# Kernel optimization log

Hardware: AMD Instinct MI355X
Metric: run time of the kernel (lower is better)

The kernel has to match this reference:

```python
import jax, jax.numpy as jnp
import numpy as np

KSIZE = 7
HEAD_DIM = 64
EPS = 1e-6

def rmsnorm(x, w):
    return x * jax.lax.rsqrt(jnp.mean(x * x, axis=-1, keepdims=True) + EPS) * w

def rope2d(x):
    # Split channels: first half rotated by row position, second half by column position.
    B, H, W, C = x.shape
    half = C // 2
    q = half // 2
    inv = 1.0 / (10000.0 ** (jnp.arange(q, dtype=jnp.float32) / q))
    th_y = jnp.arange(H, dtype=jnp.float32)[:, None] * inv  # [H,q]
    th_x = jnp.arange(W, dtype=jnp.float32)[:, None] * inv  # [W,q]
    def rot(v, th):  # v: [...,q,2], th broadcastable to [...,q]
        c, s = jnp.cos(th), jnp.sin(th)
        a, b = v[..., 0], v[..., 1]
        return jnp.stack([a * c - b * s, a * s + b * c], axis=-1)
    xy = rot(x[..., :half].reshape(B, H, W, q, 2), th_y[None, :, None, :])
    xx = rot(x[..., half:].reshape(B, H, W, q, 2), th_x[None, None, :, :])
    return jnp.concatenate([xy.reshape(B, H, W, half), xx.reshape(B, H, W, half)], axis=-1)

def neighborhood_attn(x, w_qkv, w_proj, b_proj, k=KSIZE, hd=HEAD_DIM):
    # NATTEN semantics: each query attends to a k x k window; window start is
    # clamped at borders so every query sees exactly k*k keys.
    B, H, W, C = x.shape
    nh = C // hd
    qkv = x @ w_qkv                           # [B,H,W,3C]
    qv, kv, vv = jnp.split(qkv, 3, axis=-1)
    qh = qv.reshape(B, H, W, nh, hd)
    kh = kv.reshape(B, H, W, nh, hd)
    vh = vv.reshape(B, H, W, nh, hd)
    idx_h = jnp.clip(jnp.arange(H) - k // 2, 0, H - k)[:, None] + jnp.arange(k)  # [H,k]
    idx_w = jnp.clip(jnp.arange(W) - k // 2, 0, W - k)[:, None] + jnp.arange(k)  # [W,k]
    def gather(t):  # [B,H,W,nh,hd] -> [B,H,W,nh,k*k,hd]
        g = t[:, idx_h]            # [B,H,k,W,nh,hd]
        g = g[:, :, :, idx_w]      # [B,H,k,W,k,nh,hd]
        return g.transpose(0, 1, 3, 5, 2, 4, 6).reshape(B, H, W, nh, k * k, hd)
    kn = gather(kh)
    vn = gather(vh)
    scale = 1.0 / np.sqrt(hd).astype(np.float32)
    logits = jnp.einsum('bxynd,bxynkd->bxynk', qh, kn) * scale
    attn = jax.nn.softmax(logits, axis=-1)
    out = jnp.einsum('bxynk,bxynkd->bxynd', attn, vn).reshape(B, H, W, C)
    return out @ w_proj + b_proj

def geglu(x, ff1_w, ff1_b, ff2_w, ff2_b):
    h = x @ ff1_w + ff1_b
    gate, value = jnp.split(h, 2, axis=-1)
    return (jax.nn.gelu(gate, approximate=False) * value) @ ff2_w + ff2_b

def setup_inputs():
    key = jax.random.key(0)
    B, H, W, C = 2, 64, 64, 256
    ks = jax.random.split(key, 8)
    g = lambda k, shape, sc: jax.random.normal(k, shape, jnp.float32) * sc
    return {
        'x': g(ks[0], (B, H, W, C), 1.0),
        'norm1_w': jnp.ones((C,), jnp.float32),
        'norm2_w': jnp.ones((C,), jnp.float32),
        'w_qkv': g(ks[1], (C, 3 * C), 0.02),
        'w_proj': g(ks[2], (C, C), 0.02),
        'b_proj': g(ks[3], (C,), 0.02),
        'ff1_w': g(ks[4], (C, 2 * C), 0.02),
        'ff1_b': g(ks[5], (2 * C,), 0.02),
        'ff2_w': g(ks[6], (C, C), 0.02),
        'ff2_b': g(ks[7], (C,), 0.02),
    }

def reference(x, norm1_w, norm2_w, w_qkv, w_proj, b_proj, ff1_w, ff1_b, ff2_w, ff2_b):
    h = rope2d(rmsnorm(x, norm1_w))
    x = x + neighborhood_attn(h, w_qkv, w_proj, b_proj)
    x = x + geglu(rmsnorm(x, norm2_w), ff1_w, ff1_b, ff2_w, ff2_b)
    return x
```

## Files before the change

kernel.cpp:

```cpp
#include <hip/hip_runtime.h>
#include <hip/hip_bf16.h>


#define ROWS 8192
typedef unsigned int uint32;
typedef unsigned short ushort16;
typedef __attribute__((ext_vector_type(8))) short short8;
typedef __attribute__((ext_vector_type(4))) float floatx4;

__device__ __forceinline__ float bf2f(__hip_bfloat16 b) { return __bfloat162float(b); }
__device__ __forceinline__ float us2f(ushort16 u) {
    return __uint_as_float(((uint32)u) << 16);
}
__device__ __forceinline__ ushort16 f2us(float f) {
    __hip_bfloat16 h = __float2bfloat16(f);
    return *(ushort16*)&h;
}
__device__ __forceinline__ float ldflag(const void* p, size_t i, int f32) {
    return f32 ? ((const float*)p)[i] : bf2f(((const __hip_bfloat16*)p)[i]);
}

__device__ __forceinline__ void gl_lds16(const void* gptr, void* lptr) {
    __builtin_amdgcn_global_load_lds(
        (const __attribute__((address_space(1))) uint32*)gptr,
        (__attribute__((address_space(3))) uint32*)lptr, 16, 0, 0);
}

__global__ __launch_bounds__(64) void detect_kernel(const ushort16* __restrict__ xu,
                                                    int* __restrict__ flag) {
    const int lane = threadIdx.x;
    const float v = us2f(xu[lane * 62]);
    const float a = fabsf(v);
    const bool sane = (a < 1e4f) && (a > 1e-8f);
    const unsigned long long m = __ballot(sane);
    if (lane == 0) flag[0] = (__popcll(m) < 32) ? 1 : 0;
}

struct WSrc {
    const void *wqkv, *wproj, *ff1w, *ff2w, *bproj, *ff1b, *ff2b;
};
__global__ __launch_bounds__(256) void cvt_kernel(WSrc s, ushort16* __restrict__ wT,
                                                  float* __restrict__ bF,
                                                  const int* __restrict__ flag) {
    const int f32 = flag[0];
    const int bid = blockIdx.x, tid = threadIdx.x;
    if (bid == 112) {
        #pragma unroll
        for (int it = 0; it < 4; ++it) {
            const int j = it * 256 + tid;
            float v;
            if (j < 256)      v = ldflag(s.bproj, j, f32);
            else if (j < 768) v = ldflag(s.ff1b, j - 256, f32);
            else              v = ldflag(s.ff2b, j - 768, f32);
            bF[j] = v;
        }
        return;
    }
    const void* src; int N, kt, nt, base;
    if (bid < 48)      { src = s.wqkv;  N = 768; kt = bid / 12;      nt = bid % 12;      base = 0; }
    else if (bid < 64) { const int l = bid - 48; src = s.wproj; N = 256; kt = l / 4; nt = l % 4; base = 196608; }
    else if (bid < 96) { const int l = bid - 64; src = s.ff1w;  N = 512; kt = l / 8; nt = l % 8; base = 262144; }
    else               { const int l = bid - 96; src = s.ff2w;  N = 256; kt = l / 4; nt = l % 4; base = 393216; }

    __shared__ ushort16 T[64][65];
    const int r0 = tid >> 6, c = tid & 63;
    #pragma unroll
    for (int j = 0; j < 16; ++j) {
        const int r = j * 4 + r0;
        T[r][c] = f2us(ldflag(src, (size_t)(kt * 64 + r) * N + nt * 64 + c, f32));
    }
    __syncthreads();
    const int n = tid >> 2, kg = tid & 3;
    #pragma unroll
    for (int j = 0; j < 16; ++j) {
        const int k = kg * 16 + j;
        wT[base + (size_t)(nt * 64 + n) * 256 + kt * 64 + k] = T[k][n];
    }
}

__global__ __launch_bounds__(256) void rms1_kernel(const void* __restrict__ in,
                                                   const void* __restrict__ w,
                                                   ushort16* __restrict__ out,
                                                   const int* __restrict__ flag) {
    const int f32 = flag[0];
    const int wid = threadIdx.x >> 6, lane = threadIdx.x & 63;
    const int row = blockIdx.x * 4 + wid;
    const int c0 = lane * 4;
    const size_t base = (size_t)row * 256 + c0;

    float v[4];
    if (f32) {
        const float4 d = *(const float4*)((const float*)in + base);
        v[0] = d.x; v[1] = d.y; v[2] = d.z; v[3] = d.w;
    } else {
        const ushort4 d = *(const ushort4*)((const ushort16*)in + base);
        v[0] = us2f(d.x); v[1] = us2f(d.y); v[2] = us2f(d.z); v[3] = us2f(d.w);
    }

    float sq = v[0] * v[0] + v[1] * v[1] + v[2] * v[2] + v[3] * v[3];
    #pragma unroll
    for (int off = 32; off; off >>= 1) sq += __shfl_xor(sq, off);
    const float rr = rsqrtf(sq * (1.0f / 256.0f) + 1e-6f);

    float nv[4];
    #pragma unroll
    for (int i = 0; i < 4; ++i) nv[i] = v[i] * rr * ldflag(w, c0 + i, f32);

    const int py = (row >> 6) & 63, px = row & 63;
    const float pos = (c0 < 128) ? (float)py : (float)px;
    const int j0 = (c0 & 127) >> 1;
    #pragma unroll
    for (int p = 0; p < 2; ++p) {
        const float inv = expf(-(float)(j0 + p) * (9.210340371976184f / 64.0f));
        const float th = pos * inv;
        const float cs = cosf(th), sn = sinf(th);
        const float a = nv[p * 2], b = nv[p * 2 + 1];
        nv[p * 2]     = a * cs - b * sn;
        nv[p * 2 + 1] = a * sn + b * cs;
    }
    ushort4 o;
    o.x = f2us(nv[0]); o.y = f2us(nv[1]); o.z = f2us(nv[2]); o.w = f2us(nv[3]);
    *(ushort4*)(out + base) = o;
}

template <int BM, int BN, int WR, int WC, int EPI>
__global__ __launch_bounds__(256) void gemm_mfma(const ushort16* __restrict__ A,
                                                 const ushort16* __restrict__ Bt,
                                                 const float* __restrict__ bias,
                                                 const void* __restrict__ resid,
                                                 void* __restrict__ Cout,
                                                 int N, const int* __restrict__ flag) {
    constexpr int TM = BM / (WR * 16), TN = BN / (WC * 16);
    constexpr int CHA = BM / 16, CHT = (BM + BN) / 16;
    __shared__ ushort16 At[BM * 32];
    __shared__ ushort16 Bs[BN * 32];

    const int f32 = flag[0];
    const int tid = threadIdx.x, lane = tid & 63, wid = tid >> 6;
    const int wr = wid / WC, wc = wid % WC;
    const int m0 = blockIdx.y * BM, n0 = blockIdx.x * BN;
    const int mw = wr * TM * 16, nw = wc * TN * 16;
    const int cr = lane >> 2, cc = (lane & 3) * 8;
    const int l15 = lane & 15, kq = (lane >> 4) * 8;

    floatx4 acc[TM][TN] = {};

    for (int k0 = 0; k0 < 256; k0 += 32) {
        #pragma unroll
        for (int c = 0; c < CHT / 4 + 1; ++c) {
            const int ch = wid + c * 4;
            if (ch < CHT) {
                const ushort16* g;
                ushort16* l;
                if (ch < CHA) {
                    g = A + (size_t)(m0 + ch * 16 + cr) * 256 + k0 + cc;
                    l = At + ch * 512;
                } else {
                    const int c2 = ch - CHA;
                    g = Bt + (size_t)(n0 + c2 * 16 + cr) * 256 + k0 + cc;
                    l = Bs + c2 * 512;
                }
                gl_lds16(g, l);
            }
        }
        __syncthreads();

        short8 af[TM], bf[TN];
        #pragma unroll
        for (int mi = 0; mi < TM; ++mi)
            af[mi] = *(const short8*)&At[(mw + mi * 16 + l15) * 32 + kq];
        #pragma unroll
        for (int nj = 0; nj < TN; ++nj)
            bf[nj] = *(const short8*)&Bs[(nw + nj * 16 + l15) * 32 + kq];
        #pragma unroll
        for (int mi = 0; mi < TM; ++mi)
            #pragma unroll
            for (int nj = 0; nj < TN; ++nj)
                acc[mi][nj] = __builtin_amdgcn_mfma_f32_16x16x32_bf16(af[mi], bf[nj], acc[mi][nj], 0, 0, 0);
        __syncthreads();
    }

    const int crow = (lane >> 4) * 4;
    #pragma unroll
    for (int mi = 0; mi < TM; ++mi) {
        #pragma unroll
        for (int nj = 0; nj < TN; ++nj) {
            const int n = n0 + nw + nj * 16 + l15;
            const float bs = (EPI > 0) ? bias[n] : 0.0f;
            #pragma unroll
            for (int r = 0; r < 4; ++r) {
                const int m = m0 + mw + mi * 16 + crow + r;
                const size_t oi = (size_t)m * N + n;
                float v = acc[mi][nj][r] + bs;
                if (EPI == 3) v += ((const float*)resid)[oi];
                if (EPI == 0) {
                    ((ushort16*)Cout)[oi] = f2us(v);
                } else {
                    if (f32) ((float*)Cout)[oi] = v;
                    else     ((ushort16*)Cout)[oi] = f2us(v);
                }
            }
        }
    }
}

__global__ __launch_bounds__(256) void gemm_proj_rms(const ushort16* __restrict__ A,
                                                     const ushort16* __restrict__ Bt,
                                                     const float* __restrict__ bias,
                                                     const void* __restrict__ xres,
                                                     const void* __restrict__ n2w,
                                                     float* __restrict__ x1,
                                                     ushort16* __restrict__ y,
                                                     const int* __restrict__ flag) {
    constexpr int TM = 2, TN = 4;
    __shared__ ushort16 At[32 * 32];
    __shared__ ushort16 Bs[256 * 32];
    __shared__ float red[4][32];

    const int f32 = flag[0];
    const int tid = threadIdx.x, lane = tid & 63, wid = tid >> 6;
    const int m0 = blockIdx.x * 32;
    const int nw = wid * 64;
    const int cr = lane >> 2, cc = (lane & 3) * 8;
    const int l15 = lane & 15, kq = (lane >> 4) * 8;

    floatx4 acc[TM][TN] = {};

    for (int k0 = 0; k0 < 256; k0 += 32) {
        #pragma unroll
        for (int c = 0; c < 5; ++c) {
            const int ch = wid + c * 4;
            if (ch < 18) {
                const ushort16* g;
                ushort16* l;
                if (ch < 2) {
                    g = A + (size_t)(m0 + ch * 16 + cr) * 256 + k0 + cc;
                    l = At + ch * 512;
                } else {
                    const int c2 = ch - 2;
                    g = Bt + (size_t)(c2 * 16 + cr) * 256 + k0 + cc;
                    l = Bs + c2 * 512;
                }
                gl_lds16(g, l);
            }
        }
        __syncthreads();

        short8 af[TM], bf[TN];
        #pragma unroll
        for (int mi = 0; mi < TM; ++mi)
            af[mi] = *(const short8*)&At[(mi * 16 + l15) * 32 + kq];
        #pragma unroll
        for (int nj = 0; nj < TN; ++nj)
            bf[nj] = *(const short8*)&Bs[(nw + nj * 16 + l15) * 32 + kq];
        #pragma unroll
        for (int mi = 0; mi < TM; ++mi)
            #pragma unroll
            for (int nj = 0; nj < TN; ++nj)
                acc[mi][nj] = __builtin_amdgcn_mfma_f32_16x16x32_bf16(af[mi], bf[nj], acc[mi][nj], 0, 0, 0);
        __syncthreads();
    }

    const int crow = (lane >> 4) * 4;
    float w2[TN], bsv[TN];
    #pragma unroll
    for (int nj = 0; nj < TN; ++nj) {
        const int n = nw + nj * 16 + l15;
        w2[nj] = ldflag(n2w, n, f32);
        bsv[nj] = bias[n];
    }

    float ps[TM][4] = {};
    #pragma unroll
    for (int mi = 0; mi < TM; ++mi)
        #pragma unroll
        for (int nj = 0; nj < TN; ++nj)
            #pragma unroll
            for (int r = 0; r < 4; ++r) {
                const int m = m0 + mi * 16 + crow + r;
                const int n = nw + nj * 16 + l15;
                float v = acc[mi][nj][r] + bsv[nj] + ldflag(xres, (size_t)m * 256 + n, f32);
                acc[mi][nj][r] = v;
                ps[mi][r] += v * v;
            }
    #pragma unroll
    for (int off = 1; off < 16; off <<= 1)
        #pragma unroll
        for (int mi = 0; mi < TM; ++mi)
            #pragma unroll
            for (int r = 0; r < 4; ++r) ps[mi][r] += __shfl_xor(ps[mi][r], off);
    if (l15 == 0)
        #pragma unroll
        for (int mi = 0; mi < TM; ++mi)
            #pragma unroll
            for (int r = 0; r < 4; ++r) red[wid][mi * 16 + crow + r] = ps[mi][r];
    __syncthreads();

    float rr[TM][4];
    #pragma unroll
    for (int mi = 0; mi < TM; ++mi)
        #pragma unroll
        for (int r = 0; r < 4; ++r) {
            const int row = mi * 16 + crow + r;
            const float s = red[0][row] + red[1][row] + red[2][row] + red[3][row];
            rr[mi][r] = rsqrtf(s * (1.0f / 256.0f) + 1e-6f);
        }
    #pragma unroll
    for (int mi = 0; mi < TM; ++mi)
        #pragma unroll
        for (int nj = 0; nj < TN; ++nj)
            #pragma unroll
            for (int r = 0; r < 4; ++r) {
                const int m = m0 + mi * 16 + crow + r;
                const int n = nw + nj * 16 + l15;
                const size_t oi = (size_t)m * 256 + n;
                const float v = acc[mi][nj][r];
                x1[oi] = v;
                y[oi] = f2us(v * rr[mi][r] * w2[nj]);
            }
}

__global__ __launch_bounds__(256) void gemm_ff1_geglu(const ushort16* __restrict__ A,
                                                      const ushort16* __restrict__ Bt,
                                                      const float* __restrict__ bF,
                                                      ushort16* __restrict__ g,
                                                      const int* __restrict__ flag) {
    constexpr int TM = 2, TN = 4;
    __shared__ ushort16 At[128 * 32];
    __shared__ ushort16 Bg[64 * 32];
    __shared__ ushort16 Bv[64 * 32];

    const int tid = threadIdx.x, lane = tid & 63, wid = tid >> 6;
    const int m0 = blockIdx.y * 128, ng0 = blockIdx.x * 64;
    const int mw = wid * 32;
    const int cr = lane >> 2, cc = (lane & 3) * 8;
    const int l15 = lane & 15, kq = (lane >> 4) * 8;

    floatx4 accg[TM][TN] = {}, accv[TM][TN] = {};

    for (int k0 = 0; k0 < 256; k0 += 32) {
        #pragma unroll
        for (int c = 0; c < 4; ++c) {
            const int ch = wid + c * 4;
            const ushort16* gp;
            ushort16* l;
            if (ch < 8) {
                gp = A + (size_t)(m0 + ch * 16 + cr) * 256 + k0 + cc;
                l = At + ch * 512;
            } else if (ch < 12) {
                const int c2 = ch - 8;
                gp = Bt + (size_t)(ng0 + c2 * 16 + cr) * 256 + k0 + cc;
                l = Bg + c2 * 512;
            } else {
                const int c2 = ch - 12;
                gp = Bt + (size_t)(ng0 + 256 + c2 * 16 + cr) * 256 + k0 + cc;
                l = Bv + c2 * 512;
            }
            gl_lds16(gp, l);
        }
        __syncthreads();

        short8 af[TM], bg[TN], bv[TN];
        #pragma unroll
        for (int mi = 0; mi < TM; ++mi)
            af[mi] = *(const short8*)&At[(mw + mi * 16 + l15) * 32 + kq];
        #pragma unroll
        for (int nj = 0; nj < TN; ++nj) {
            bg[nj] = *(const short8*)&Bg[(nj * 16 + l15) * 32 + kq];
            bv[nj] = *(const short8*)&Bv[(nj * 16 + l15) * 32 + kq];
        }
        #pragma unroll
        for (int mi = 0; mi < TM; ++mi)
            #pragma unroll
            for (int nj = 0; nj < TN; ++nj) {
                accg[mi][nj] = __builtin_amdgcn_mfma_f32_16x16x32_bf16(af[mi], bg[nj], accg[mi][nj], 0, 0, 0);
                accv[mi][nj] = __builtin_amdgcn_mfma_f32_16x16x32_bf16(af[mi], bv[nj], accv[mi][nj], 0, 0, 0);
            }
        __syncthreads();
    }

    const int crow = (lane >> 4) * 4;
    #pragma unroll
    for (int mi = 0; mi < TM; ++mi) {
        #pragma unroll
        for (int nj = 0; nj < TN; ++nj) {
            const int n = ng0 + nj * 16 + l15;
            const float bg_ = bF[256 + n], bv_ = bF[512 + n];
            #pragma unroll
            for (int r = 0; r < 4; ++r) {
                const int m = m0 + mw + mi * 16 + crow + r;
                const float gate = accg[mi][nj][r] + bg_;
                const float val = accv[mi][nj][r] + bv_;
                const float ge = 0.5f * gate * (1.0f + erff(gate * 0.70710678118654752f));
                g[(size_t)m * 256 + n] = f2us(ge * val);
            }
        }
    }
}

__global__ __launch_bounds__(256) void attn_kernel(const ushort16* __restrict__ qkv,
                                                   ushort16* __restrict__ ao) {
    __shared__ ushort16 smem[40208];
    ushort16* const KS = smem;
    ushort16* const VT = smem + 12544;
    ushort16* const PL = smem + 26880;

    const int tid = threadIdx.x, lane = tid & 63, wid = tid >> 6;
    const int l15 = lane & 15, kq8 = (lane >> 4) * 8;
    const int bid = blockIdx.x;
    const int h = bid & 3;
    const int t = (bid >> 2) & 63;
    const int b = bid >> 8;
    const int ty0 = (t >> 3) * 8, tx0 = (t & 7) * 8;
    const int hby = min(max(ty0 - 3, 0), 50);
    const int hbx = min(max(tx0 - 3, 0), 50);
    const int hcol = h * 64;

    const int qpl = wid * 16 + l15;
    const int qpy = ty0 + (qpl >> 3), qpx = tx0 + (qpl & 7);
    const size_t qoff = (size_t)(b * 4096 + qpy * 64 + qpx) * 768 + hcol + kq8;
    const short8 af0 = *(const short8*)&qkv[qoff];
    const short8 af1 = *(const short8*)&qkv[qoff + 32];

    for (int it = tid; it < 3136; it += 256) {
        const bool isK = it < 1568;
        const int task = isK ? it : it - 1568;
        const int key = task >> 3, oct = task & 7;
        const int pix = b * 4096 + (hby + key / 14) * 64 + hbx + key % 14;
        const uint4 d = *(const uint4*)&qkv[(size_t)pix * 768 + (isK ? 256 : 512) + hcol + oct * 8];
        if (isK) {
            uint32* dst = (uint32*)&KS[(oct >> 2) * 6272 + key * 32 + (oct & 3) * 8];
            dst[0] = d.x; dst[1] = d.y; dst[2] = d.z; dst[3] = d.w;
        } else {
            const ushort16* s8 = (const ushort16*)&d;
            #pragma unroll
            for (int j = 0; j < 8; ++j) VT[(oct * 8 + j) * 224 + key] = s8[j];
        }
    }
    for (int it = tid; it < 1792; it += 256)
        VT[(it / 28) * 224 + 196 + (it % 28)] = 0;
    __syncthreads();

    floatx4 acc[13];
    #pragma unroll
    for (int nt = 0; nt < 13; ++nt) {
        const int krow = (nt * 16 + l15) * 32 + kq8;
        const short8 bf0 = *(const short8*)&KS[krow];
        const short8 bf1 = *(const short8*)&KS[6272 + krow];
        floatx4 a = {0.0f, 0.0f, 0.0f, 0.0f};
        a = __builtin_amdgcn_mfma_f32_16x16x32_bf16(af0, bf0, a, 0, 0, 0);
        a = __builtin_amdgcn_mfma_f32_16x16x32_bf16(af1, bf1, a, 0, 0, 0);
        acc[nt] = a;
    }

    int kyA[13], kxA[13];
    #pragma unroll
    for (int nt = 0; nt < 13; ++nt) {
        const int kidx = nt * 16 + l15;
        kyA[nt] = hby + kidx / 14;
        kxA[nt] = hbx + kidx % 14;
    }

    const int crow = (lane >> 4) * 4;
    float rs[4];
    #pragma unroll
    for (int r = 0; r < 4; ++r) {
        const int pl = wid * 16 + crow + r;
        const int py = ty0 + (pl >> 3), px = tx0 + (pl & 7);
        const int sy = min(max(py - 3, 0), 57), sx = min(max(px - 3, 0), 57);
        float lv[13];
        float mx = -1e30f;
        #pragma unroll
        for (int nt = 0; nt < 13; ++nt) {
            const int kidx = nt * 16 + l15;
            const bool valid = (kidx < 196) &&
                               ((unsigned)(kyA[nt] - sy) < 7u) &&
                               ((unsigned)(kxA[nt] - sx) < 7u);
            lv[nt] = valid ? acc[nt][r] * 0.125f : -1e30f;
            mx = fmaxf(mx, lv[nt]);
        }
        #pragma unroll
        for (int off = 1; off < 16; off <<= 1) mx = fmaxf(mx, __shfl_xor(mx, off));
        float sme = 0.0f;
        #pragma unroll
        for (int nt = 0; nt < 13; ++nt) {
            const float e = exp2f((lv[nt] - mx) * 1.4426950408889634f);
            lv[nt] = e;
            sme += e;
        }
        #pragma unroll
        for (int off = 1; off < 16; off <<= 1) sme += __shfl_xor(sme, off);
        rs[r] = 1.0f / sme;
        #pragma unroll
        for (int nt = 0; nt < 13; ++nt)
            PL[pl * 208 + nt * 16 + l15] = f2us(lv[nt]);
    }
    __syncthreads();

    floatx4 oacc[4] = {};
    #pragma unroll
    for (int kc = 0; kc < 7; ++kc) {
        const short8 af = *(const short8*)&PL[(wid * 16 + l15) * 208 + kc * 32 + kq8];
        #pragma unroll
        for (int nd = 0; nd < 4; ++nd) {
            const short8 bf = *(const short8*)&VT[(nd * 16 + l15) * 224 + kc * 32 + kq8];
            oacc[nd] = __builtin_amdgcn_mfma_f32_16x16x32_bf16(af, bf, oacc[nd], 0, 0, 0);
        }
    }
    #pragma unroll
    for (int r = 0; r < 4; ++r) {
        const int pl = wid * 16 + crow + r;
        const int py = ty0 + (pl >> 3), px = tx0 + (pl & 7);
        const size_t o = (size_t)(b * 4096 + py * 64 + px) * 256 + hcol;
        #pragma unroll
        for (int nd = 0; nd < 4; ++nd)
            ao[o + nd * 16 + l15] = f2us(oacc[nd][r] * rs[r]);
    }
}

extern "C" void kernel_launch(void* const* d_in, const int* in_sizes, int n_in,
                              void* d_out, int out_size, void* d_ws, size_t ws_size,
                              hipStream_t stream) {
    const void* x   = d_in[0];
    const void* n1w = d_in[1];
    const void* n2w = d_in[2];
    WSrc ws_src{d_in[3], d_in[4], d_in[6], d_in[8], d_in[5], d_in[7], d_in[9]};

    char* ws = (char*)d_ws;
    int*      flag = (int*)ws;
    ushort16* wT   = (ushort16*)(ws + 4096);
    float*    bF   = (float*)(ws + 4096 + 458752 * 2);
    ushort16* h    = (ushort16*)(ws + (1 << 20));
    ushort16* qkv  = (ushort16*)(ws + (5 << 20));
    ushort16* ao   = (ushort16*)(ws + (size_t)(17 << 20));
    float*    x1   = (float*)(ws + (size_t)(21 << 20));

    ushort16* wqkvT  = wT;
    ushort16* wprojT = wT + 196608;
    ushort16* ff1wT  = wT + 262144;
    ushort16* ff2wT  = wT + 393216;

    detect_kernel<<<1, 64, 0, stream>>>((const ushort16*)x, flag);
    cvt_kernel<<<113, 256, 0, stream>>>(ws_src, wT, bF, flag);
    rms1_kernel<<<2048, 256, 0, stream>>>(x, n1w, h, flag);
    gemm_mfma<128, 128, 2, 2, 0><<<dim3(6, 64), 256, 0, stream>>>(h, wqkvT, nullptr, nullptr, qkv, 768, flag);
    attn_kernel<<<512, 256, 0, stream>>>(qkv, ao);
    gemm_proj_rms<<<256, 256, 0, stream>>>(ao, wprojT, bF, x, n2w, x1, h, flag);
    gemm_ff1_geglu<<<dim3(4, 64), 256, 0, stream>>>(h, ff1wT, bF, ao, flag);
    gemm_mfma<64, 128, 1, 4, 3><<<dim3(2, 128), 256, 0, stream>>>(ao, ff2wT, bF + 768, x1, d_out, 256, flag);
}
```

Baseline: 153.6 us.

## Fuse RMSNorm+RoPE into QKV GEMM and FF1-GEGLU-FF2 into one kernel

```diff
diff --git a/kernel.cpp b/kernel.cpp
--- a/kernel.cpp
+++ b/kernel.cpp
@@ -78,129 +78,224 @@
     }
 }
 
-__global__ __launch_bounds__(256) void rms1_kernel(const void* __restrict__ in,
-                                                   const void* __restrict__ w,
-                                                   ushort16* __restrict__ out,
-                                                   const int* __restrict__ flag) {
-    const int f32 = flag[0];
-    const int wid = threadIdx.x >> 6, lane = threadIdx.x & 63;
-    const int row = blockIdx.x * 4 + wid;
-    const int c0 = lane * 4;
-    const size_t base = (size_t)row * 256 + c0;
-
-    float v[4];
-    if (f32) {
-        const float4 d = *(const float4*)((const float*)in + base);
-        v[0] = d.x; v[1] = d.y; v[2] = d.z; v[3] = d.w;
-    } else {
-        const ushort4 d = *(const ushort4*)((const ushort16*)in + base);
-        v[0] = us2f(d.x); v[1] = us2f(d.y); v[2] = us2f(d.z); v[3] = us2f(d.w);
-    }
-
-    float sq = v[0] * v[0] + v[1] * v[1] + v[2] * v[2] + v[3] * v[3];
-    #pragma unroll
-    for (int off = 32; off; off >>= 1) sq += __shfl_xor(sq, off);
-    const float rr = rsqrtf(sq * (1.0f / 256.0f) + 1e-6f);
-
-    float nv[4];
-    #pragma unroll
-    for (int i = 0; i < 4; ++i) nv[i] = v[i] * rr * ldflag(w, c0 + i, f32);
-
-    const int py = (row >> 6) & 63, px = row & 63;
-    const float pos = (c0 < 128) ? (float)py : (float)px;
-    const int j0 = (c0 & 127) >> 1;
-    #pragma unroll
-    for (int p = 0; p < 2; ++p) {
-        const float inv = expf(-(float)(j0 + p) * (9.210340371976184f / 64.0f));
-        const float th = pos * inv;
-        const float cs = cosf(th), sn = sinf(th);
-        const float a = nv[p * 2], b = nv[p * 2 + 1];
-        nv[p * 2]     = a * cs - b * sn;
-        nv[p * 2 + 1] = a * sn + b * cs;
-    }
-    ushort4 o;
-    o.x = f2us(nv[0]); o.y = f2us(nv[1]); o.z = f2us(nv[2]); o.w = f2us(nv[3]);
-    *(ushort4*)(out + base) = o;
-}
-
-template <int BM, int BN, int WR, int WC, int EPI>
-__global__ __launch_bounds__(256) void gemm_mfma(const ushort16* __restrict__ A,
-                                                 const ushort16* __restrict__ Bt,
-                                                 const float* __restrict__ bias,
-                                                 const void* __restrict__ resid,
-                                                 void* __restrict__ Cout,
-                                                 int N, const int* __restrict__ flag) {
-    constexpr int TM = BM / (WR * 16), TN = BN / (WC * 16);
-    constexpr int CHA = BM / 16, CHT = (BM + BN) / 16;
-    __shared__ ushort16 At[BM * 32];
-    __shared__ ushort16 Bs[BN * 32];
+__global__ __launch_bounds__(256) void fused_qkv(const void* __restrict__ x,
+                                                 const void* __restrict__ n1w,
+                                                 const ushort16* __restrict__ wqkvT,
+                                                 ushort16* __restrict__ qkv,
+                                                 const int* __restrict__ flag) {
+    __shared__ ushort16 Apad[32 * 264];
+    __shared__ ushort16 Bs[256 * 32];
 
     const int f32 = flag[0];
     const int tid = threadIdx.x, lane = tid & 63, wid = tid >> 6;
-    const int wr = wid / WC, wc = wid % WC;
-    const int m0 = blockIdx.y * BM, n0 = blockIdx.x * BN;
-    const int mw = wr * TM * 16, nw = wc * TN * 16;
+    const int l15 = lane & 15, kq8 = (lane >> 4) * 8;
+    const int n0 = blockIdx.x * 256, m0 = blockIdx.y * 32;
+    const int nw = wid * 64;
     const int cr = lane >> 2, cc = (lane & 3) * 8;
-    const int l15 = lane & 15, kq = (lane >> 4) * 8;
-
-    floatx4 acc[TM][TN] = {};
-
+
+    {
+        const int row = tid >> 3, s = tid & 7;
+        const int gm = m0 + row;
+        float v[32];
+        #pragma unroll
+        for (int j = 0; j < 8; ++j) {
+            const size_t off = (size_t)gm * 256 + s * 32 + j * 4;
+            if (f32) {
+                const float4 d = *(const float4*)((const float*)x + off);
+                v[j * 4] = d.x; v[j * 4 + 1] = d.y; v[j * 4 + 2] = d.z; v[j * 4 + 3] = d.w;
+            } else {
+                const ushort4 d = *(const ushort4*)((const ushort16*)x + off);
+                v[j * 4] = us2f(d.x); v[j * 4 + 1] = us2f(d.y);
+                v[j * 4 + 2] = us2f(d.z); v[j * 4 + 3] = us2f(d.w);
+            }
+        }
+        float sq = 0.0f;
+        #pragma unroll
+        for (int i = 0; i < 32; ++i) sq += v[i] * v[i];
+        sq += __shfl_xor(sq, 1);
+        sq += __shfl_xor(sq, 2);
+        sq += __shfl_xor(sq, 4);
+        const float rr = rsqrtf(sq * (1.0f / 256.0f) + 1e-6f);
+
+        const int py = (gm >> 6) & 63, px = gm & 63;
+        #pragma unroll
+        for (int j = 0; j < 8; ++j) {
+            const int c0 = s * 32 + j * 4;
+            float nv[4];
+            #pragma unroll
+            for (int u = 0; u < 4; ++u)
+                nv[u] = v[j * 4 + u] * rr * ldflag(n1w, c0 + u, f32);
+            const float pos = (c0 < 128) ? (float)py : (float)px;
+            const int j0 = (c0 & 127) >> 1;
+            #pragma unroll
+            for (int p = 0; p < 2; ++p) {
+                const float inv = expf(-(float)(j0 + p) * (9.210340371976184f / 64.0f));
+                const float th = pos * inv;
+                const float cs = cosf(th), sn = sinf(th);
+                const float a = nv[p * 2], b = nv[p * 2 + 1];
+                nv[p * 2]     = a * cs - b * sn;
+                nv[p * 2 + 1] = a * sn + b * cs;
+            }
+            ushort4 o;
+            o.x = f2us(nv[0]); o.y = f2us(nv[1]); o.z = f2us(nv[2]); o.w = f2us(nv[3]);
+            *(ushort4*)&Apad[row * 264 + c0] = o;
+        }
+    }
+    __syncthreads();
+
+    floatx4 acc[2][4] = {};
     for (int k0 = 0; k0 < 256; k0 += 32) {
         #pragma unroll
-        for (int c = 0; c < CHT / 4 + 1; ++c) {
+        for (int c = 0; c < 4; ++c) {
             const int ch = wid + c * 4;
-            if (ch < CHT) {
-                const ushort16* g;
-                ushort16* l;
-                if (ch < CHA) {
-                    g = A + (size_t)(m0 + ch * 16 + cr) * 256 + k0 + cc;
-                    l = At + ch * 512;
-                } else {
-                    const int c2 = ch - CHA;
-                    g = Bt + (size_t)(n0 + c2 * 16 + cr) * 256 + k0 + cc;
-                    l = Bs + c2 * 512;
-                }
-                gl_lds16(g, l);
-            }
-        }
-        __syncthreads();
-
-        short8 af[TM], bf[TN];
-        #pragma unroll
-        for (int mi = 0; mi < TM; ++mi)
-            af[mi] = *(const short8*)&At[(mw + mi * 16 + l15) * 32 + kq];
-        #pragma unroll
-        for (int nj = 0; nj < TN; ++nj)
-            bf[nj] = *(const short8*)&Bs[(nw + nj * 16 + l15) * 32 + kq];
-        #pragma unroll
-        for (int mi = 0; mi < TM; ++mi)
-            #pragma unroll
-            for (int nj = 0; nj < TN; ++nj)
+            gl_lds16(wqkvT + (size_t)(n0 + ch * 16 + cr) * 256 + k0 + cc, Bs + ch * 512);
+        }
+        __syncthreads();
+        short8 af[2], bf[4];
+        #pragma unroll
+        for (int mi = 0; mi < 2; ++mi)
+            af[mi] = *(const short8*)&Apad[(mi * 16 + l15) * 264 + k0 + kq8];
+        #pragma unroll
+        for (int nj = 0; nj < 4; ++nj)
+            bf[nj] = *(const short8*)&Bs[(nw + nj * 16 + l15) * 32 + kq8];
+        #pragma unroll
+        for (int mi = 0; mi < 2; ++mi)
+            #pragma unroll
+            for (int nj = 0; nj < 4; ++nj)
                 acc[mi][nj] = __builtin_amdgcn_mfma_f32_16x16x32_bf16(af[mi], bf[nj], acc[mi][nj], 0, 0, 0);
         __syncthreads();
     }
 
     const int crow = (lane >> 4) * 4;
     #pragma unroll
-    for (int mi = 0; mi < TM; ++mi) {
-        #pragma unroll
-        for (int nj = 0; nj < TN; ++nj) {
-            const int n = n0 + nw + nj * 16 + l15;
-            const float bs = (EPI > 0) ? bias[n] : 0.0f;
+    for (int mi = 0; mi < 2; ++mi)
+        #pragma unroll
+        for (int nj = 0; nj < 4; ++nj)
             #pragma unroll
             for (int r = 0; r < 4; ++r) {
-                const int m = m0 + mw + mi * 16 + crow + r;
-                const size_t oi = (size_t)m * N + n;
-                float v = acc[mi][nj][r] + bs;
-                if (EPI == 3) v += ((const float*)resid)[oi];
-                if (EPI == 0) {
-                    ((ushort16*)Cout)[oi] = f2us(v);
-                } else {
-                    if (f32) ((float*)Cout)[oi] = v;
-                    else     ((ushort16*)Cout)[oi] = f2us(v);
-                }
-            }
-        }
+                const int m = m0 + mi * 16 + crow + r;
+                const int n = n0 + nw + nj * 16 + l15;
+                qkv[(size_t)m * 768 + n] = f2us(acc[mi][nj][r]);
+            }
+}
+
+__global__ __launch_bounds__(256) void attn_kernel(const ushort16* __restrict__ qkv,
+                                                   ushort16* __restrict__ ao) {
+    __shared__ ushort16 smem[40208];
+    ushort16* const KS = smem;
+    ushort16* const VT = smem + 12544;
+    ushort16* const PL = smem + 26880;
+
+    const int tid = threadIdx.x, lane = tid & 63, wid = tid >> 6;
+    const int l15 = lane & 15, kq8 = (lane >> 4) * 8;
+    const int bid = blockIdx.x;
+    const int h = bid & 3;
+    const int t = (bid >> 2) & 63;
+    const int b = bid >> 8;
+    const int ty0 = (t >> 3) * 8, tx0 = (t & 7) * 8;
+    const int hby = min(max(ty0 - 3, 0), 50);
+    const int hbx = min(max(tx0 - 3, 0), 50);
+    const int hcol = h * 64;
+
+    const int qpl = wid * 16 + l15;
+    const int qpy = ty0 + (qpl >> 3), qpx = tx0 + (qpl & 7);
+    const size_t qoff = (size_t)(b * 4096 + qpy * 64 + qpx) * 768 + hcol + kq8;
+    const short8 af0 = *(const short8*)&qkv[qoff];
+    const short8 af1 = *(const short8*)&qkv[qoff + 32];
+
+    for (int it = tid; it < 3136; it += 256) {
+        const bool isK = it < 1568;
+        const int task = isK ? it : it - 1568;
+        const int key = task >> 3, oct = task & 7;
+        const int pix = b * 4096 + (hby + key / 14) * 64 + hbx + key % 14;
+        const uint4 d = *(const uint4*)&qkv[(size_t)pix * 768 + (isK ? 256 : 512) + hcol + oct * 8];
+        if (isK) {
+            uint32* dst = (uint32*)&KS[(oct >> 2) * 6272 + key * 32 + (oct & 3) * 8];
+            dst[0] = d.x; dst[1] = d.y; dst[2] = d.z; dst[3] = d.w;
+        } else {
+            const ushort16* s8 = (const ushort16*)&d;
+            #pragma unroll
+            for (int j = 0; j < 8; ++j) VT[(oct * 8 + j) * 224 + key] = s8[j];
+        }
+    }
+    for (int it = tid; it < 1792; it += 256)
+        VT[(it / 28) * 224 + 196 + (it % 28)] = 0;
+    __syncthreads();
+
+    floatx4 acc[13];
+    #pragma unroll
+    for (int nt = 0; nt < 13; ++nt) {
+        const int krow = (nt * 16 + l15) * 32 + kq8;
+        const short8 bf0 = *(const short8*)&KS[krow];
+        const short8 bf1 = *(const short8*)&KS[6272 + krow];
+        floatx4 a = {0.0f, 0.0f, 0.0f, 0.0f};
+        a = __builtin_amdgcn_mfma_f32_16x16x32_bf16(af0, bf0, a, 0, 0, 0);
+        a = __builtin_amdgcn_mfma_f32_16x16x32_bf16(af1, bf1, a, 0, 0, 0);
+        acc[nt] = a;
+    }
+
+    int kyA[13], kxA[13];
+    #pragma unroll
+    for (int nt = 0; nt < 13; ++nt) {
+        const int kidx = nt * 16 + l15;
+        kyA[nt] = hby + kidx / 14;
+        kxA[nt] = hbx + kidx % 14;
+    }
+
+    const int crow = (lane >> 4) * 4;
+    float rs[4];
+    #pragma unroll
+    for (int r = 0; r < 4; ++r) {
+        const int pl = wid * 16 + crow + r;
+        const int py = ty0 + (pl >> 3), px = tx0 + (pl & 7);
+        const int sy = min(max(py - 3, 0), 57), sx = min(max(px - 3, 0), 57);
+        float lv[13];
+        float mx = -1e30f;
+        #pragma unroll
+        for (int nt = 0; nt < 13; ++nt) {
+            const int kidx = nt * 16 + l15;
+            const bool valid = (kidx < 196) &&
+                               ((unsigned)(kyA[nt] - sy) < 7u) &&
+                               ((unsigned)(kxA[nt] - sx) < 7u);
+            lv[nt] = valid ? acc[nt][r] * 0.125f : -1e30f;
+            mx = fmaxf(mx, lv[nt]);
+        }
+        #pragma unroll
+        for (int off = 1; off < 16; off <<= 1) mx = fmaxf(mx, __shfl_xor(mx, off));
+        float sme = 0.0f;
+        #pragma unroll
+        for (int nt = 0; nt < 13; ++nt) {
+            const float e = exp2f((lv[nt] - mx) * 1.4426950408889634f);
+            lv[nt] = e;
+            sme += e;
+        }
+        #pragma unroll
+        for (int off = 1; off < 16; off <<= 1) sme += __shfl_xor(sme, off);
+        rs[r] = 1.0f / sme;
+        #pragma unroll
+        for (int nt = 0; nt < 13; ++nt)
+            PL[pl * 208 + nt * 16 + l15] = f2us(lv[nt]);
+    }
+    __syncthreads();
+
+    floatx4 oacc[4] = {};
+    #pragma unroll
+    for (int kc = 0; kc < 7; ++kc) {
+        const short8 af = *(const short8*)&PL[(wid * 16 + l15) * 208 + kc * 32 + kq8];
+        #pragma unroll
+        for (int nd = 0; nd < 4; ++nd) {
+            const short8 bf = *(const short8*)&VT[(nd * 16 + l15) * 224 + kc * 32 + kq8];
+            oacc[nd] = __builtin_amdgcn_mfma_f32_16x16x32_bf16(af, bf, oacc[nd], 0, 0, 0);
+        }
+    }
+    #pragma unroll
+    for (int r = 0; r < 4; ++r) {
+        const int pl = wid * 16 + crow + r;
+        const int py = ty0 + (pl >> 3), px = tx0 + (pl & 7);
+        const size_t o = (size_t)(b * 4096 + py * 64 + px) * 256 + hcol;
+        #pragma unroll
+        for (int nd = 0; nd < 4; ++nd)
+            ao[o + nd * 16 + l15] = f2us(oacc[nd][r] * rs[r]);
     }
 }
 
@@ -320,202 +415,115 @@
             }
 }
 
-__global__ __launch_bounds__(256) void gemm_ff1_geglu(const ushort16* __restrict__ A,
-                                                      const ushort16* __restrict__ Bt,
-                                                      const float* __restrict__ bF,
-                                                      ushort16* __restrict__ g,
-                                                      const int* __restrict__ flag) {
-    constexpr int TM = 2, TN = 4;
-    __shared__ ushort16 At[128 * 32];
-    __shared__ ushort16 Bg[64 * 32];
-    __shared__ ushort16 Bv[64 * 32];
-
+__global__ __launch_bounds__(256) void fused_ffn(const ushort16* __restrict__ y,
+                                                 const ushort16* __restrict__ ff1wT,
+                                                 const ushort16* __restrict__ ff2wT,
+                                                 const float* __restrict__ bF,
+                                                 const float* __restrict__ x1,
+                                                 void* __restrict__ out,
+                                                 const int* __restrict__ flag) {
+    __shared__ ushort16 Apad[32 * 264];
+    __shared__ ushort16 Bs[512 * 32];
+
+    const int f32 = flag[0];
     const int tid = threadIdx.x, lane = tid & 63, wid = tid >> 6;
-    const int m0 = blockIdx.y * 128, ng0 = blockIdx.x * 64;
-    const int mw = wid * 32;
+    const int l15 = lane & 15, kq8 = (lane >> 4) * 8;
+    const int m0 = blockIdx.x * 32;
     const int cr = lane >> 2, cc = (lane & 3) * 8;
-    const int l15 = lane & 15, kq = (lane >> 4) * 8;
-
-    floatx4 accg[TM][TN] = {}, accv[TM][TN] = {};
-
+    const int crow = (lane >> 4) * 4;
+
+    {
+        const int row = tid >> 3, s = tid & 7;
+        #pragma unroll
+        for (int j = 0; j < 4; ++j) {
+            const int c = s * 32 + j * 8;
+            const uint4 d = *(const uint4*)&y[(size_t)(m0 + row) * 256 + c];
+            *(uint4*)&Apad[row * 264 + c] = d;
+        }
+    }
+    __syncthreads();
+
+    floatx4 accg[2][4] = {}, accv[2][4] = {};
     for (int k0 = 0; k0 < 256; k0 += 32) {
         #pragma unroll
-        for (int c = 0; c < 4; ++c) {
+        for (int c = 0; c < 8; ++c) {
             const int ch = wid + c * 4;
-            const ushort16* gp;
-            ushort16* l;
-            if (ch < 8) {
-                gp = A + (size_t)(m0 + ch * 16 + cr) * 256 + k0 + cc;
-                l = At + ch * 512;
-            } else if (ch < 12) {
-                const int c2 = ch - 8;
-                gp = Bt + (size_t)(ng0 + c2 * 16 + cr) * 256 + k0 + cc;
-                l = Bg + c2 * 512;
-            } else {
-                const int c2 = ch - 12;
-                gp = Bt + (size_t)(ng0 + 256 + c2 * 16 + cr) * 256 + k0 + cc;
-                l = Bv + c2 * 512;
-            }
-            gl_lds16(gp, l);
-        }
-        __syncthreads();
-
-        short8 af[TM], bg[TN], bv[TN];
-        #pragma unroll
-        for (int mi = 0; mi < TM; ++mi)
-            af[mi] = *(const short8*)&At[(mw + mi * 16 + l15) * 32 + kq];
-        #pragma unroll
-        for (int nj = 0; nj < TN; ++nj) {
-            bg[nj] = *(const short8*)&Bg[(nj * 16 + l15) * 32 + kq];
-            bv[nj] = *(const short8*)&Bv[(nj * 16 + l15) * 32 + kq];
-        }
-        #pragma unroll
-        for (int mi = 0; mi < TM; ++mi)
-            #pragma unroll
-            for (int nj = 0; nj < TN; ++nj) {
+            gl_lds16(ff1wT + (size_t)(ch * 16 + cr) * 256 + k0 + cc, Bs + ch * 512);
+        }
+        __syncthreads();
+        short8 af[2], bg[4], bv[4];
+        #pragma unroll
+        for (int mi = 0; mi < 2; ++mi)
+            af[mi] = *(const short8*)&Apad[(mi * 16 + l15) * 264 + k0 + kq8];
+        #pragma unroll
+        for (int nj = 0; nj < 4; ++nj) {
+            bg[nj] = *(const short8*)&Bs[(wid * 64 + nj * 16 + l15) * 32 + kq8];
+            bv[nj] = *(const short8*)&Bs[(256 + wid * 64 + nj * 16 + l15) * 32 + kq8];
+        }
+        #pragma unroll
+        for (int mi = 0; mi < 2; ++mi)
+            #pragma unroll
+            for (int nj = 0; nj < 4; ++nj) {
                 accg[mi][nj] = __builtin_amdgcn_mfma_f32_16x16x32_bf16(af[mi], bg[nj], accg[mi][nj], 0, 0, 0);
                 accv[mi][nj] = __builtin_amdgcn_mfma_f32_16x16x32_bf16(af[mi], bv[nj], accv[mi][nj], 0, 0, 0);
             }
         __syncthreads();
     }
 
-    const int crow = (lane >> 4) * 4;
-    #pragma unroll
-    for (int mi = 0; mi < TM; ++mi) {
-        #pragma unroll
-        for (int nj = 0; nj < TN; ++nj) {
-            const int n = ng0 + nj * 16 + l15;
+    #pragma unroll
+    for (int mi = 0; mi < 2; ++mi)
+        #pragma unroll
+        for (int nj = 0; nj < 4; ++nj) {
+            const int n = wid * 64 + nj * 16 + l15;
             const float bg_ = bF[256 + n], bv_ = bF[512 + n];
             #pragma unroll
             for (int r = 0; r < 4; ++r) {
-                const int m = m0 + mw + mi * 16 + crow + r;
                 const float gate = accg[mi][nj][r] + bg_;
                 const float val = accv[mi][nj][r] + bv_;
                 const float ge = 0.5f * gate * (1.0f + erff(gate * 0.70710678118654752f));
-                g[(size_t)m * 256 + n] = f2us(ge * val);
-            }
-        }
-    }
-}
-
-__global__ __launch_bounds__(256) void attn_kernel(const ushort16* __restrict__ qkv,
-                                                   ushort16* __restrict__ ao) {
-    __shared__ ushort16 smem[40208];
-    ushort16* const KS = smem;
-    ushort16* const VT = smem + 12544;
-    ushort16* const PL = smem + 26880;
-
-    const int tid = threadIdx.x, lane = tid & 63, wid = tid >> 6;
-    const int l15 = lane & 15, kq8 = (lane >> 4) * 8;
-    const int bid = blockIdx.x;
-    const int h = bid & 3;
-    const int t = (bid >> 2) & 63;
-    const int b = bid >> 8;
-    const int ty0 = (t >> 3) * 8, tx0 = (t & 7) * 8;
-    const int hby = min(max(ty0 - 3, 0), 50);
-    const int hbx = min(max(tx0 - 3, 0), 50);
-    const int hcol = h * 64;
-
-    const int qpl = wid * 16 + l15;
-    const int qpy = ty0 + (qpl >> 3), qpx = tx0 + (qpl & 7);
-    const size_t qoff = (size_t)(b * 4096 + qpy * 64 + qpx) * 768 + hcol + kq8;
-    const short8 af0 = *(const short8*)&qkv[qoff];
-    const short8 af1 = *(const short8*)&qkv[qoff + 32];
-
-    for (int it = tid; it < 3136; it += 256) {
-        const bool isK = it < 1568;
-        const int task = isK ? it : it - 1568;
-        const int key = task >> 3, oct = task & 7;
-        const int pix = b * 4096 + (hby + key / 14) * 64 + hbx + key % 14;
-        const uint4 d = *(const uint4*)&qkv[(size_t)pix * 768 + (isK ? 256 : 512) + hcol + oct * 8];
-        if (isK) {
-            uint32* dst = (uint32*)&KS[(oct >> 2) * 6272 + key * 32 + (oct & 3) * 8];
-            dst[0] = d.x; dst[1] = d.y; dst[2] = d.z; dst[3] = d.w;
-        } else {
-            const ushort16* s8 = (const ushort16*)&d;
-            #pragma unroll
-            for (int j = 0; j < 8; ++j) VT[(oct * 8 + j) * 224 + key] = s8[j];
-        }
-    }
-    for (int it = tid; it < 1792; it += 256)
-        VT[(it / 28) * 224 + 196 + (it % 28)] = 0;
-    __syncthreads();
-
-    floatx4 acc[13];
-    #pragma unroll
-    for (int nt = 0; nt < 13; ++nt) {
-        const int krow = (nt * 16 + l15) * 32 + kq8;
-        const short8 bf0 = *(const short8*)&KS[krow];
-        const short8 bf1 = *(const short8*)&KS[6272 + krow];
-        floatx4 a = {0.0f, 0.0f, 0.0f, 0.0f};
-        a = __builtin_amdgcn_mfma_f32_16x16x32_bf16(af0, bf0, a, 0, 0, 0);
-        a = __builtin_amdgcn_mfma_f32_16x16x32_bf16(af1, bf1, a, 0, 0, 0);
-        acc[nt] = a;
-    }
-
-    int kyA[13], kxA[13];
-    #pragma unroll
-    for (int nt = 0; nt < 13; ++nt) {
-        const int kidx = nt * 16 + l15;
-        kyA[nt] = hby + kidx / 14;
-        kxA[nt] = hbx + kidx % 14;
-    }
-
-    const int crow = (lane >> 4) * 4;
-    float rs[4];
-    #pragma unroll
-    for (int r = 0; r < 4; ++r) {
-        const int pl = wid * 16 + crow + r;
-        const int py = ty0 + (pl >> 3), px = tx0 + (pl & 7);
-        const int sy = min(max(py - 3, 0), 57), sx = min(max(px - 3, 0), 57);
-        float lv[13];
-        float mx = -1e30f;
-        #pragma unroll
-        for (int nt = 0; nt < 13; ++nt) {
-            const int kidx = nt * 16 + l15;
-            const bool valid = (kidx < 196) &&
-                               ((unsigned)(kyA[nt] - sy) < 7u) &&
-                               ((unsigned)(kxA[nt] - sx) < 7u);
-            lv[nt] = valid ? acc[nt][r] * 0.125f : -1e30f;
-            mx = fmaxf(mx, lv[nt]);
-        }
-        #pragma unroll
-        for (int off = 1; off < 16; off <<= 1) mx = fmaxf(mx, __shfl_xor(mx, off));
-        float sme = 0.0f;
-        #pragma unroll
-        for (int nt = 0; nt < 13; ++nt) {
-            const float e = exp2f((lv[nt] - mx) * 1.4426950408889634f);
-            lv[nt] = e;
-            sme += e;
-        }
-        #pragma unroll
-        for (int off = 1; off < 16; off <<= 1) sme += __shfl_xor(sme, off);
-        rs[r] = 1.0f / sme;
-        #pragma unroll
-        for (int nt = 0; nt < 13; ++nt)
-            PL[pl * 208 + nt * 16 + l15] = f2us(lv[nt]);
-    }
-    __syncthreads();
-
-    floatx4 oacc[4] = {};
-    #pragma unroll
-    for (int kc = 0; kc < 7; ++kc) {
-        const short8 af = *(const short8*)&PL[(wid * 16 + l15) * 208 + kc * 32 + kq8];
-        #pragma unroll
-        for (int nd = 0; nd < 4; ++nd) {
-            const short8 bf = *(const short8*)&VT[(nd * 16 + l15) * 224 + kc * 32 + kq8];
-            oacc[nd] = __builtin_amdgcn_mfma_f32_16x16x32_bf16(af, bf, oacc[nd], 0, 0, 0);
-        }
-    }
-    #pragma unroll
-    for (int r = 0; r < 4; ++r) {
-        const int pl = wid * 16 + crow + r;
-        const int py = ty0 + (pl >> 3), px = tx0 + (pl & 7);
-        const size_t o = (size_t)(b * 4096 + py * 64 + px) * 256 + hcol;
-        #pragma unroll
-        for (int nd = 0; nd < 4; ++nd)
-            ao[o + nd * 16 + l15] = f2us(oacc[nd][r] * rs[r]);
-    }
+                Apad[(mi * 16 + crow + r) * 264 + n] = f2us(ge * val);
+            }
+        }
+    __syncthreads();
+
+    floatx4 acc2[2][4] = {};
+    for (int k0 = 0; k0 < 256; k0 += 32) {
+        #pragma unroll
+        for (int c = 0; c < 4; ++c) {
+            const int ch = wid + c * 4;
+            gl_lds16(ff2wT + (size_t)(ch * 16 + cr) * 256 + k0 + cc, Bs + ch * 512);
+        }
+        __syncthreads();
+        short8 af[2], bf[4];
+        #pragma unroll
+        for (int mi = 0; mi < 2; ++mi)
+            af[mi] = *(const short8*)&Apad[(mi * 16 + l15) * 264 + k0 + kq8];
+        #pragma unroll
+        for (int nj = 0; nj < 4; ++nj)
+            bf[nj] = *(const short8*)&Bs[(wid * 64 + nj * 16 + l15) * 32 + kq8];
+        #pragma unroll
+        for (int mi = 0; mi < 2; ++mi)
+            #pragma unroll
+            for (int nj = 0; nj < 4; ++nj)
+                acc2[mi][nj] = __builtin_amdgcn_mfma_f32_16x16x32_bf16(af[mi], bf[nj], acc2[mi][nj], 0, 0, 0);
+        __syncthreads();
+    }
+
+    #pragma unroll
+    for (int mi = 0; mi < 2; ++mi)
+        #pragma unroll
+        for (int nj = 0; nj < 4; ++nj) {
+            const int n = wid * 64 + nj * 16 + l15;
+            const float bs = bF[768 + n];
+            #pragma unroll
+            for (int r = 0; r < 4; ++r) {
+                const int m = m0 + mi * 16 + crow + r;
+                const size_t oi = (size_t)m * 256 + n;
+                const float v = acc2[mi][nj][r] + bs + x1[oi];
+                if (f32) ((float*)out)[oi] = v;
+                else     ((ushort16*)out)[oi] = f2us(v);
+            }
+        }
 }
 
 extern "C" void kernel_launch(void* const* d_in, const int* in_sizes, int n_in,
@@ -530,7 +538,7 @@
     int*      flag = (int*)ws;
     ushort16* wT   = (ushort16*)(ws + 4096);
     float*    bF   = (float*)(ws + 4096 + 458752 * 2);
-    ushort16* h    = (ushort16*)(ws + (1 << 20));
+    ushort16* y    = (ushort16*)(ws + (1 << 20));
     ushort16* qkv  = (ushort16*)(ws + (5 << 20));
     ushort16* ao   = (ushort16*)(ws + (size_t)(17 << 20));
     float*    x1   = (float*)(ws + (size_t)(21 << 20));
@@ -542,10 +550,8 @@
 
     detect_kernel<<<1, 64, 0, stream>>>((const ushort16*)x, flag);
     cvt_kernel<<<113, 256, 0, stream>>>(ws_src, wT, bF, flag);
-    rms1_kernel<<<2048, 256, 0, stream>>>(x, n1w, h, flag);
-    gemm_mfma<128, 128, 2, 2, 0><<<dim3(6, 64), 256, 0, stream>>>(h, wqkvT, nullptr, nullptr, qkv, 768, flag);
+    fused_qkv<<<dim3(3, 256), 256, 0, stream>>>(x, n1w, wqkvT, qkv, flag);
     attn_kernel<<<512, 256, 0, stream>>>(qkv, ao);
-    gemm_proj_rms<<<256, 256, 0, stream>>>(ao, wprojT, bF, x, n2w, x1, h, flag);
-    gemm_ff1_geglu<<<dim3(4, 64), 256, 0, stream>>>(h, ff1wT, bF, ao, flag);
-    gemm_mfma<64, 128, 1, 4, 3><<<dim3(2, 128), 256, 0, stream>>>(ao, ff2wT, bF + 768, x1, d_out, 256, flag);
-}
+    gemm_proj_rms<<<256, 256, 0, stream>>>(ao, wprojT, bF, x, n2w, x1, y, flag);
+    fused_ffn<<<256, 256, 0, stream>>>(y, ff1wT, ff2wT, bF, x1, d_out, flag);
+}
```

Result: no change. 156.2 us (+1.7%).
